# Kernel tuning notes

Hardware: AMD Instinct MI355X
Metric: run time of the kernel (lower is better)

Reference implementation:

```python
import jax, jax.numpy as jnp
import numpy as np

D_MODEL, D_INNER, D_CONV, D_STATE, DT_RANK = 1024, 2048, 4, 16, 64
B_SZ, L = 2, 2048


def setup_inputs() -> dict:
    key = jax.random.key(0)
    ks = jax.random.split(key, 8)
    s = 0.02
    x = jax.random.normal(ks[0], (B_SZ, L, D_MODEL), jnp.float32)
    in_proj_w = jax.random.normal(ks[1], (D_MODEL, 2 * D_INNER), jnp.float32) * s
    conv_w = jax.random.normal(ks[2], (D_INNER, 1, D_CONV), jnp.float32) * 0.1
    conv_b = jax.random.normal(ks[3], (D_INNER,), jnp.float32) * 0.1
    x_proj_w = jax.random.normal(ks[4], (D_INNER, DT_RANK + 2 * D_STATE), jnp.float32) * s
    dt_proj_w = jax.random.normal(ks[5], (DT_RANK, D_INNER), jnp.float32) * s
    dt_proj_b = jax.random.normal(ks[6], (D_INNER,), jnp.float32) * 0.1
    A_log = jnp.log(jnp.broadcast_to(jnp.arange(1, D_STATE + 1, dtype=jnp.float32), (D_INNER, D_STATE)))
    D = jnp.ones((D_INNER,), jnp.float32)
    out_proj_w = jax.random.normal(ks[7], (D_INNER, D_MODEL), jnp.float32) * s
    return dict(x=x, in_proj_w=in_proj_w, conv_w=conv_w, conv_b=conv_b,
                x_proj_w=x_proj_w, dt_proj_w=dt_proj_w, dt_proj_b=dt_proj_b,
                A_log=A_log, D=D, out_proj_w=out_proj_w)


def _selective_scan(u, delta, A, B, C, D):
    # u, delta: (b,l,d); A: (d,n); B,C: (b,l,n); D: (d,)
    b, l, d = u.shape
    n = A.shape[1]
    deltaA = jnp.exp(jnp.einsum('bld,dn->bldn', delta, A))          # (b,l,d,n)
    deltaB_u = jnp.einsum('bld,bln,bld->bldn', delta, B, u)          # (b,l,d,n)

    def step(xc, inputs):
        dA_t, dBu_t, C_t = inputs                                     # (b,d,n),(b,d,n),(b,n)
        xc = dA_t * xc + dBu_t
        y_t = jnp.einsum('bdn,bn->bd', xc, C_t)
        return xc, y_t

    x0 = jnp.zeros((b, d, n), u.dtype)
    _, ys = jax.lax.scan(step, x0, (deltaA.transpose(1, 0, 2, 3),
                                    deltaB_u.transpose(1, 0, 2, 3),
                                    C.transpose(1, 0, 2)))
    return ys.transpose(1, 0, 2) + u * D


def reference(x, in_proj_w, conv_w, conv_b, x_proj_w, dt_proj_w, dt_proj_b, A_log, D, out_proj_w):
    b, l, _ = x.shape
    xr = x @ in_proj_w                                                # (b,l,2*d_inner)
    xi, res = jnp.split(xr, 2, axis=-1)
    # causal depthwise conv1d (torch pads both sides by d_conv-1 then slices [:l])
    xc = jax.lax.conv_general_dilated(
        xi.transpose(0, 2, 1), conv_w, window_strides=(1,),
        padding=[(D_CONV - 1, 0)], feature_group_count=D_INNER,
        dimension_numbers=('NCH', 'OIH', 'NCH')) + conv_b[None, :, None]
    xc = jax.nn.silu(xc.transpose(0, 2, 1))                           # (b,l,d_inner)
    # SSM
    A = -jnp.exp(A_log)
    x_dbl = xc @ x_proj_w                                             # (b,l,dt_rank+2n)
    dt, Bm, Cm = jnp.split(x_dbl, [DT_RANK, DT_RANK + D_STATE], axis=-1)
    delta = jax.nn.softplus(dt @ dt_proj_w + dt_proj_b)               # (b,l,d_inner)
    y = _selective_scan(xc, delta, A, Bm, Cm, D)
    y = y * jax.nn.silu(res)
    return y @ out_proj_w
```

## Files before the change

### kernel.cpp

```cpp
#include <hip/hip_runtime.h>
#include <hip/hip_bf16.h>

#define D_MODEL 1024
#define D_INNER 2048
#define D_CONV  4
#define D_STATE 16
#define DT_RANK 64
#define B_SZ    2
#define SEQ_L   2048
#define BLROWS  (B_SZ * SEQ_L)

#define NCHUNK  64
#define CHUNK   (SEQ_L / NCHUNK)

#define XP_N    96
#define XP_SPLIT 8
#define XP_KCH  (D_INNER / XP_SPLIT)

typedef __hip_bfloat16 bf16;
typedef __attribute__((ext_vector_type(8))) short bshort8;
typedef __attribute__((ext_vector_type(4))) float f32x4;

__device__ __forceinline__ float b2f(bf16 v) { return __bfloat162float(v); }
__device__ __forceinline__ bf16  f2b(float v) { return __float2bfloat16(v); }
__device__ __forceinline__ short f2s(float v) {
    bf16 h = __float2bfloat16(v);
    return *reinterpret_cast<short*>(&h);
}
__device__ __forceinline__ float s2f(short s) {
    unsigned u = ((unsigned)(unsigned short)s) << 16;
    float f; __builtin_memcpy(&f, &u, 4); return f;
}
__device__ __forceinline__ float siluf(float x) { return x / (1.f + __expf(-x)); }
__device__ __forceinline__ float softplusf(float x) {
    return fmaxf(x, 0.f) + log1pf(__expf(-fabsf(x)));
}
__device__ __forceinline__ float exp_neg(float a) { return __expf(fminf(a, 0.f)); }

__device__ __forceinline__ void gl2lds16(const bf16* g, bf16* l) {
    __builtin_amdgcn_global_load_lds((const __attribute__((address_space(1))) void*)g,
                                     (__attribute__((address_space(3))) void*)l,
                                     16, 0, 0);
}

#define N_X    (B_SZ * SEQ_L * D_MODEL)
#define N_IPW  (D_MODEL * 2 * D_INNER)
#define N_CW   (D_INNER * D_CONV)
#define N_CB   (D_INNER)
#define N_XPW  (D_INNER * (DT_RANK + 2*D_STATE))
#define N_DTW  (DT_RANK * D_INNER)
#define N_DTB  (D_INNER)
#define N_AL   (D_INNER * D_STATE)
#define N_D    (D_INNER)
#define N_OPW  (D_INNER * D_MODEL)

#define S0 ((long)N_X)
#define S1 (S0 + N_IPW)
#define S2 (S1 + N_CW)
#define S3 (S2 + N_CB)
#define S4 (S3 + N_XPW)
#define S5 (S4 + N_DTW)
#define S6 (S5 + N_DTB)
#define S7 (S6 + N_AL)
#define S8 (S7 + N_D)
#define S9 (S8 + N_OPW)

#define PP_CVT   1024
#define PP_T0    4096
#define PP_T1    192
#define PP_T2    128
#define PP_T3    2048
#define PP_TOTAL (PP_CVT + PP_T0 + PP_T1 + PP_T2 + PP_T3)

__global__ __launch_bounds__(256)
void preprocess_kernel(int* __restrict__ flag,
                       const void* p0, const void* p1, const void* p2,
                       const void* p3, const void* p4, const void* p5,
                       const void* p6, const void* p7, const void* p8,
                       const void* p9,
                       bf16* __restrict__ canon,
                       bf16* __restrict__ d_ipw, bf16* __restrict__ d_xpw,
                       bf16* __restrict__ d_dtw, bf16* __restrict__ d_opw)
{
    __shared__ float tile[32][33];
    const float* al = (const float*)p7;
    const bool f32 = (fabsf(al[1] - 0.6931472f) < 0.05f) && (fabsf(al[0]) < 1e-3f);

    if (blockIdx.x == 0 && threadIdx.x == 0) {
        int fast = f32 ? 1 : 0;
        if (f32) {
            const int rows[3] = {0, 513, 1023};
            for (int i = 0; i < 3 && fast; ++i)
                for (int n = 0; n < D_STATE; ++n)
                    if (fabsf(al[rows[i] * D_STATE + n] - logf((float)(n + 1))) > 2e-3f)
                        { fast = 0; break; }
        }
        flag[0] = f32 ? 1 : 0;
        flag[1] = fast;
    }

    int bid = blockIdx.x;
    if (bid < PP_CVT) {
        const long total4 = S9 / 4;
        for (long i4 = (long)bid * 256 + threadIdx.x; i4 < total4;
             i4 += (long)PP_CVT * 256) {
            long idx = i4 * 4;
            const void* src; long lo; bool keep = true;
            if      (idx < S0) { src = p0; lo = idx; }
            else if (idx < S1) { src = p1; lo = idx - S0; keep = false; }
            else if (idx < S2) { src = p2; lo = idx - S1; }
            else if (idx < S3) { src = p3; lo = idx - S2; }
            else if (idx < S4) { src = p4; lo = idx - S3; keep = false; }
            else if (idx < S5) { src = p5; lo = idx - S4; keep = false; }
            else if (idx < S6) { src = p6; lo = idx - S5; }
            else if (idx < S7) { src = p7; lo = idx - S6; }
            else if (idx < S8) { src = p8; lo = idx - S7; }
            else               { src = p9; lo = idx - S8; keep = false; }
            if (!keep) continue;
            ushort4 o;
            if (f32) {
                float4 v = ((const float4*)src)[lo >> 2];
                o.x = (unsigned short)f2s(v.x); o.y = (unsigned short)f2s(v.y);
                o.z = (unsigned short)f2s(v.z); o.w = (unsigned short)f2s(v.w);
            } else {
                o = ((const ushort4*)src)[lo >> 2];
            }
            ((ushort4*)canon)[idx >> 2] = o;
        }
        return;
    }

    bid -= PP_CVT;
    const void* src; bf16* dst; int R, C, txt;
    if (bid < PP_T0)      { src = p1; dst = d_ipw; R = D_MODEL; C = 2 * D_INNER; txt = 128; }
    else if ((bid -= PP_T0) < PP_T1) { src = p4; dst = d_xpw; R = D_INNER; C = XP_N;    txt = 3;  }
    else if ((bid -= PP_T1) < PP_T2) { src = p5; dst = d_dtw; R = DT_RANK; C = D_INNER; txt = 64; }
    else                  { bid -= PP_T2; src = p9; dst = d_opw; R = D_INNER; C = D_MODEL; txt = 32; }

    const int r0 = (bid / txt) * 32, c0 = (bid % txt) * 32;
    const int tx = threadIdx.x & 31, ty = threadIdx.x >> 5;

    #pragma unroll
    for (int p = 0; p < 4; ++p) {
        int r = r0 + ty + p * 8, c = c0 + tx;
        float v = 0.f;
        if (r < R && c < C)
            v = f32 ? ((const float*)src)[(size_t)r * C + c]
                    : b2f(((const bf16*)src)[(size_t)r * C + c]);
        tile[ty + p * 8][tx] = v;
    }
    __syncthreads();
    #pragma unroll
    for (int p = 0; p < 4; ++p) {
        int c = c0 + ty + p * 8, r = r0 + tx;
        if (c < C && r < R)
            dst[(size_t)c * R + r] = f2b(tile[tx][ty + p * 8]);
    }
}

#define IP_NT (D_MODEL / 64)

#define IP_STA(nb, k0n, s)                                                    \
    { _Pragma("unroll") for (int c = 0; c < 2; ++c) {                         \
        const int rr = aR + (s) * 64 + c * 8;                                 \
        gl2lds16(A + (size_t)(row0 + rr + lr) * D_MODEL + (k0n) + slot * 8,   \
                 &As[nb][rr * 64]); } }

#define IP_STB(nb, k0n, s)                                                    \
    { _Pragma("unroll") for (int c = 0; c < 2; ++c) {                         \
        const int rr = bR + (s) * 16 + c * 8;                                 \
        gl2lds16(BT + (size_t)(col0 + rr + lr) * D_MODEL + (k0n) + slot * 8,  \
                 &Bs[nb][rr * 64]); } }

#define IP_LDB(cb)                                                            \
    { _Pragma("unroll") for (int j = 0; j < 4; ++j) {                         \
        bF[j][0] = *(const bshort8*)&Bs[cb][(wn*64 + j*16 + t15)*64 + fc0];   \
        bF[j][1] = *(const bshort8*)&Bs[cb][(wn*64 + j*16 + t15)*64 + fc1]; } }

#define IP_LDA(cb, i0)                                                        \
    { _Pragma("unroll") for (int ii = 0; ii < 2; ++ii) {                      \
        aF[ii][0] = *(const bshort8*)&As[cb][(wm*128 + ((i0)+ii)*16 + t15)*64 + fc0]; \
        aF[ii][1] = *(const bshort8*)&As[cb][(wm*128 + ((i0)+ii)*16 + t15)*64 + fc1]; } }

#define IP_MMA(i0)                                                            \
    __builtin_amdgcn_s_setprio(1);                                            \
    { _Pragma("unroll") for (int ii = 0; ii < 2; ++ii)                        \
      _Pragma("unroll") for (int j = 0; j < 4; ++j)                           \
      _Pragma("unroll") for (int h = 0; h < 2; ++h)                           \
        acc[(i0)+ii][j] = __builtin_amdgcn_mfma_f32_16x16x32_bf16(            \
            aF[ii][h], bF[j][h], acc[(i0)+ii][j], 0, 0, 0); }                 \
    __builtin_amdgcn_s_setprio(0);

__global__ __launch_bounds__(512, 2)
void gemm_inproj256_kernel(const bf16* __restrict__ A,
                           const bf16* __restrict__ BT,
                           bf16* __restrict__ C1,
                           bf16* __restrict__ C2)
{
    __shared__ __align__(16) bf16 As[2][256 * 64];
    __shared__ __align__(16) bf16 Bs[2][256 * 64];

    const int tid  = threadIdx.x;
    const int wave = tid >> 6;
    const int lane = tid & 63;
    const int t15  = lane & 15;
    const int q    = lane >> 4;
    const int wm   = wave >> 2;
    const int wn   = wave & 3;

    int wg = blockIdx.x;
    wg = (wg & 7) * 32 + (wg >> 3);
    const int row0 = (wg >> 4) * 256;
    const int col0 = (wg & 15) * 256;

    const int lr   = lane >> 3;
    const int slot = (lane & 7) ^ lr;
    const int aR   = wm * 128 + wn * 16;
    const int bR   = wn * 64  + wm * 32;
    const int x7   = t15 & 7;
    const int fc0  = ((0 + q) ^ x7) * 8;
    const int fc1  = ((4 + q) ^ x7) * 8;

    f32x4 acc[8][4] = {};
    bshort8 bF[4][2], aF[2][2];

    IP_STB(0, 0, 0); IP_STB(0, 0, 1); IP_STA(0, 0, 0); IP_STA(0, 0, 1);

    for (int t = 0; t < IP_NT - 1; ++t) {
        const int cb = t & 1, nb = cb ^ 1;
        const int k0n = (t + 1) * 64;
        asm volatile("s_waitcnt vmcnt(2)" ::: "memory");
        __builtin_amdgcn_s_barrier();
        __builtin_amdgcn_sched_barrier(0);
        IP_LDB(cb);
        IP_LDA(cb, 0);
        IP_STB(nb, k0n, 0);
        IP_MMA(0);
        IP_LDA(cb, 2);
        IP_STB(nb, k0n, 1);
        IP_MMA(2);
        asm volatile("s_waitcnt vmcnt(4)" ::: "memory");
        __builtin_amdgcn_s_barrier();
        __builtin_amdgcn_sched_barrier(0);
        IP_LDA(cb, 4);
        IP_STA(nb, k0n, 0);
        IP_MMA(4);
        IP_LDA(cb, 6);
        IP_STA(nb, k0n, 1);
        IP_MMA(6);
        asm volatile("s_waitcnt lgkmcnt(0)" ::: "memory");
    }
    {
        const int cb = (IP_NT - 1) & 1;
        asm volatile("s_waitcnt vmcnt(2)" ::: "memory");
        __builtin_amdgcn_s_barrier();
        __builtin_amdgcn_sched_barrier(0);
        IP_LDB(cb);
        IP_LDA(cb, 0); IP_MMA(0);
        IP_LDA(cb, 2); IP_MMA(2);
        asm volatile("s_waitcnt vmcnt(0)" ::: "memory");
        __builtin_amdgcn_s_barrier();
        __builtin_amdgcn_sched_barrier(0);
        IP_LDA(cb, 4); IP_MMA(4);
        IP_LDA(cb, 6); IP_MMA(6);
    }
    #pragma unroll
    for (int i = 0; i < 8; ++i) {
        #pragma unroll
        for (int j = 0; j < 4; ++j) {
            const int c_g = col0 + wn * 64 + j * 16 + t15;
            const int r_b = row0 + wm * 128 + i * 16 + q * 4;
            #pragma unroll
            for (int r = 0; r < 4; ++r) {
                const float v = acc[i][j][r];
                if (c_g < D_INNER)
                    C1[(size_t)(r_b + r) * D_INNER + c_g] = f2b(v);
                else
                    C2[(size_t)(r_b + r) * D_INNER + (c_g - D_INNER)] = f2b(v);
            }
        }
    }
}

__global__ __launch_bounds__(256)
void gemm_mfma_bt64_kernel(const bf16* __restrict__ A, int lda,
                           const bf16* __restrict__ BT, int ldb,
                           void* __restrict__ C, int ldc,
                           int M, int N, int K,
                           const bf16* __restrict__ bias, int mode,
                           const int* __restrict__ flag)
{
    __shared__ __align__(16) bf16 As[2][64 * 32];
    __shared__ __align__(16) bf16 Bs[2][128 * 32];

    const int tid  = threadIdx.x;
    const int wave = tid >> 6;
    const int lane = tid & 63;
    const int t    = lane & 15;
    const int q    = lane >> 4;
    const int wm   = wave & 1;
    const int wn   = wave >> 1;

    const int row0 = blockIdx.y * 64;
    const int col0 = blockIdx.x * 128;

    const int s_row = lane >> 2;
    const int s_col = (lane & 3) * 8;

    f32x4 acc[2][4] = {};
    const int outf32 = (mode == 2) ? flag[0] : 0;

    for (int k0 = 0; k0 < K; k0 += 64) {
        #pragma unroll
        for (int h = 0; h < 2; ++h) {
            if (wave < 2) {
                #pragma unroll
                for (int c = 0; c < 2; ++c) {
                    const bf16* g = A + (size_t)(row0 + wave * 32 + c * 16 + s_row) * lda
                                    + k0 + h * 32 + s_col;
                    gl2lds16(g, As[h] + (wave * 32 + c * 16) * 32);
                }
            } else {
                #pragma unroll
                for (int c = 0; c < 4; ++c) {
                    const bf16* g = BT + (size_t)(col0 + (wave - 2) * 64 + c * 16 + s_row) * ldb
                                    + k0 + h * 32 + s_col;
                    gl2lds16(g, Bs[h] + ((wave - 2) * 64 + c * 16) * 32);
                }
            }
        }
        __syncthreads();

        #pragma unroll
        for (int h = 0; h < 2; ++h) {
            bshort8 aF[2], bF[4];
            #pragma unroll
            for (int i = 0; i < 2; ++i)
                aF[i] = *(const bshort8*)&As[h][((wm * 32 + i * 16 + t) << 5) + (q << 3)];
            #pragma unroll
            for (int j = 0; j < 4; ++j)
                bF[j] = *(const bshort8*)&Bs[h][((wn * 64 + j * 16 + t) << 5) + (q << 3)];

            #pragma unroll
            for (int i = 0; i < 2; ++i)
                #pragma unroll
                for (int j = 0; j < 4; ++j)
                    acc[i][j] = __builtin_amdgcn_mfma_f32_16x16x32_bf16(
                                    aF[i], bF[j], acc[i][j], 0, 0, 0);
        }
        __syncthreads();
    }

    #pragma unroll
    for (int i = 0; i < 2; ++i) {
        #pragma unroll
        for (int j = 0; j < 4; ++j) {
            const int c_g = col0 + wn * 64 + j * 16 + t;
            const int r_b = row0 + wm * 32 + i * 16 + q * 4;
            #pragma unroll
            for (int r = 0; r < 4; ++r) {
                const int r_g = r_b + r;
                float v = acc[i][j][r];
                if (mode == 1) {
                    v += b2f(bias[c_g]);
                    ((bf16*)C)[(size_t)r_g * ldc + c_g] = f2b(softplusf(v));
                } else {
                    size_t o = (size_t)r_g * ldc + c_g;
                    if (outf32) ((float*)C)[o] = v;
                    else        ((bf16*)C)[o]  = f2b(v);
                }
            }
        }
    }
}

__global__ __launch_bounds__(256)
void xproj_splitk_kernel(const bf16* __restrict__ A,
                         const bf16* __restrict__ BT,
                         float* __restrict__ part)
{
    __shared__ __align__(16) bf16 As[2][128 * 32];
    __shared__ __align__(16) bf16 Bs[2][XP_N * 32];

    const int tid  = threadIdx.x;
    const int wave = tid >> 6;
    const int lane = tid & 63;
    const int t    = lane & 15;
    const int q    = lane >> 4;

    const int row0 = blockIdx.x * 128;
    const int s    = blockIdx.y;
    const int kbeg = s * XP_KCH;

    const int s_row = lane >> 2;
    const int s_col = (lane & 3) * 8;

    f32x4 acc[2][6] = {};

    for (int k0 = kbeg; k0 < kbeg + XP_KCH; k0 += 64) {
        #pragma unroll
        for (int h = 0; h < 2; ++h) {
            if (wave < 2) {
                #pragma unroll
                for (int c = 0; c < 4; ++c) {
                    const bf16* g = A + (size_t)(row0 + wave * 64 + c * 16 + s_row) * D_INNER
                                    + k0 + h * 32 + s_col;
                    gl2lds16(g, As[h] + (wave * 64 + c * 16) * 32);
                }
            } else {
                const int nb = (wave == 2) ? 4 : 2;
                for (int c = 0; c < nb; ++c) {
                    const bf16* g = BT + (size_t)((wave - 2) * 64 + c * 16 + s_row) * D_INNER
                                    + k0 + h * 32 + s_col;
                    gl2lds16(g, Bs[h] + ((wave - 2) * 64 + c * 16) * 32);
                }
            }
        }
        __syncthreads();

        #pragma unroll
        for (int h = 0; h < 2; ++h) {
            bshort8 aF[2], bF[6];
            #pragma unroll
            for (int i = 0; i < 2; ++i)
                aF[i] = *(const bshort8*)&As[h][((wave * 32 + i * 16 + t) << 5) + (q << 3)];
            #pragma unroll
            for (int j = 0; j < 6; ++j)
                bF[j] = *(const bshort8*)&Bs[h][((j * 16 + t) << 5) + (q << 3)];

            #pragma unroll
            for (int i = 0; i < 2; ++i)
                #pragma unroll
                for (int j = 0; j < 6; ++j)
                    acc[i][j] = __builtin_amdgcn_mfma_f32_16x16x32_bf16(
                                    aF[i], bF[j], acc[i][j], 0, 0, 0);
        }
        __syncthreads();
    }

    #pragma unroll
    for (int i = 0; i < 2; ++i) {
        #pragma unroll
        for (int j = 0; j < 6; ++j) {
            const int c_g = j * 16 + t;
            const int r_b = row0 + wave * 32 + i * 16 + q * 4;
            #pragma unroll
            for (int r = 0; r < 4; ++r)
                part[((size_t)s * BLROWS + (r_b + r)) * XP_N + c_g] = acc[i][j][r];
        }
    }
}

__global__ __launch_bounds__(256)
void xproj_reduce_kernel(const float* __restrict__ part, bf16* __restrict__ xdbl)
{
    int idx = blockIdx.x * 256 + threadIdx.x;
    if (idx >= BLROWS * XP_N) return;
    float v = 0.f;
    #pragma unroll
    for (int s = 0; s < XP_SPLIT; ++s)
        v += part[(size_t)s * BLROWS * XP_N + idx];
    xdbl[idx] = f2b(v);
}

__global__ __launch_bounds__(256)
void conv_silu_kernel(const bf16* __restrict__ xi,
                      const bf16* __restrict__ cw,
                      const bf16* __restrict__ cb,
                      bf16* __restrict__ xc)
{
    int idx = blockIdx.x * 256 + threadIdx.x;
    const int total = BLROWS * (D_INNER / 8);
    if (idx >= total) return;
    const int d8 = idx % (D_INNER / 8);
    const int bl = idx / (D_INNER / 8);
    const int l  = bl % SEQ_L;
    const int b  = bl / SEQ_L;
    const int d0 = d8 * 8;

    bshort8 cv[4];
    #pragma unroll
    for (int v = 0; v < 4; ++v)
        cv[v] = ((const bshort8*)(cw + (size_t)d0 * 4))[v];

    bshort8 bv = *(const bshort8*)(cb + d0);
    float acc[8];
    #pragma unroll
    for (int e = 0; e < 8; ++e) acc[e] = s2f(bv[e]);

    #pragma unroll
    for (int k = 0; k < D_CONV; ++k) {
        int tt = l + k - (D_CONV - 1);
        if (tt >= 0) {
            bshort8 xv = *(const bshort8*)(xi + ((size_t)b * SEQ_L + tt) * D_INNER + d0);
            #pragma unroll
            for (int e = 0; e < 8; ++e) {
                const int f = e * 4 + k;
                acc[e] += s2f(xv[e]) * s2f(cv[f >> 3][f & 7]);
            }
        }
    }
    bshort8 ov;
    #pragma unroll
    for (int e = 0; e < 8; ++e) {
        float a = acc[e];
        ov[e] = f2s(a * (1.f / (1.f + __expf(-a))));
    }
    *(bshort8*)(xc + (size_t)bl * D_INNER + d0) = ov;
}

__global__ __launch_bounds__(256)
void scan_p1_kernel(const bf16* delta, const bf16* xc, const bf16* xdbl,
                    const bf16* A_log,
                    float* state, float* sumdelta,
                    const int* flags)
{
    __shared__ float Bsh[CHUNK][D_STATE];
    const int tid = threadIdx.x;
    const int d = blockIdx.x * 256 + tid;
    const int c = blockIdx.y;
    const int b = blockIdx.z;
    const int row0 = b * SEQ_L + c * CHUNK;
    const int fastA = flags[1];

    for (int e = tid; e < CHUNK * D_STATE; e += 256) {
        int t = e / D_STATE, n = e % D_STATE;
        Bsh[t][n] = b2f(xdbl[(size_t)(row0 + t) * 96 + DT_RANK + n]);
    }
    __syncthreads();

    float A[D_STATE];
    if (!fastA) {
        #pragma unroll
        for (int n = 0; n < D_STATE; ++n) A[n] = -__expf(b2f(A_log[d * D_STATE + n]));
    }

    float x[D_STATE] = {};
    float S = 0.f;
    if (fastA) {
        for (int t = 0; t < CHUNK; ++t) {
            size_t r = row0 + t;
            float dt_v = b2f(delta[r * D_INNER + d]);
            float u    = b2f(xc[r * D_INNER + d]);
            float bu = dt_v * u;
            S += dt_v;
            float e1 = __expf(-fmaxf(dt_v, 0.f));
            float pw[D_STATE];
            pw[0] = e1;
            #pragma unroll
            for (int n = 1; n < D_STATE; ++n)
                pw[n] = pw[(n - 1) >> 1] * pw[n >> 1];
            #pragma unroll
            for (int n = 0; n < D_STATE; ++n)
                x[n] = pw[n] * x[n] + Bsh[t][n] * bu;
        }
    } else {
        for (int t = 0; t < CHUNK; ++t) {
            size_t r = row0 + t;
            float dt_v = b2f(delta[r * D_INNER + d]);
            float u    = b2f(xc[r * D_INNER + d]);
            float bu = dt_v * u;
            S += dt_v;
            #pragma unroll
            for (int n = 0; n < D_STATE; ++n)
                x[n] = exp_neg(dt_v * A[n]) * x[n] + Bsh[t][n] * bu;
        }
    }
    size_t o = ((size_t)(b * NCHUNK + c) * D_INNER + d) * D_STATE;
    #pragma unroll
    for (int n = 0; n < D_STATE; ++n) state[o + n] = x[n];
    sumdelta[(size_t)(b * NCHUNK + c) * D_INNER + d] = S;
}

__global__ __launch_bounds__(256)
void scan_p2_kernel(const bf16* A_log, float* state, const float* sumdelta)
{
    int idx = blockIdx.x * 256 + threadIdx.x;
    int n  = idx & (D_STATE - 1);
    int dn = idx >> 4;
    int d  = dn & (D_INNER - 1);
    int b  = dn >> 11;

    float A_n = -__expf(b2f(A_log[d * D_STATE + n]));
    float carry = 0.f;
    #pragma unroll 4
    for (int c = 0; c < NCHUNK; ++c) {
        size_t o = ((size_t)(b * NCHUNK + c) * D_INNER + d) * D_STATE + n;
        float local = state[o];
        float S = sumdelta[(size_t)(b * NCHUNK + c) * D_INNER + d];
        state[o] = carry;
        carry = exp_neg(A_n * S) * carry + local;
    }
}

__global__ __launch_bounds__(256)
void scan_p3_kernel(const bf16* delta, bf16* xc, const bf16* xdbl,
                    const bf16* res,
                    const bf16* A_log, const bf16* Dvec,
                    const float* state,
                    const int* flags)
{
    __shared__ float Bsh[CHUNK][D_STATE];
    __shared__ float Csh[CHUNK][D_STATE];
    const int tid = threadIdx.x;
    const int d = blockIdx.x * 256 + tid;
    const int c = blockIdx.y;
    const int b = blockIdx.z;
    const int row0 = b * SEQ_L + c * CHUNK;
    const int fastA = flags[1];

    for (int e = tid; e < CHUNK * 2 * D_STATE; e += 256) {
        int t = e / (2 * D_STATE), j = e % (2 * D_STATE);
        float v = b2f(xdbl[(size_t)(row0 + t) * 96 + DT_RANK + j]);
        if (j < D_STATE) Bsh[t][j] = v;
        else             Csh[t][j - D_STATE] = v;
    }
    __syncthreads();

    float A[D_STATE];
    if (!fastA) {
        #pragma unroll
        for (int n = 0; n < D_STATE; ++n) A[n] = -__expf(b2f(A_log[d * D_STATE + n]));
    }
    const float Dd = b2f(Dvec[d]);

    float x[D_STATE];
    size_t o = ((size_t)(b * NCHUNK + c) * D_INNER + d) * D_STATE;
    #pragma unroll
    for (int n = 0; n < D_STATE; ++n) x[n] = state[o + n];

    if (fastA) {
        for (int t = 0; t < CHUNK; ++t) {
            size_t r = row0 + t;
            float dt_v = b2f(delta[r * D_INNER + d]);
            float u    = b2f(xc[r * D_INNER + d]);
            float resv = b2f(res[r * D_INNER + d]);
            float bu = dt_v * u;
            float e1 = __expf(-fmaxf(dt_v, 0.f));
            float pw[D_STATE];
            pw[0] = e1;
            #pragma unroll
            for (int n = 1; n < D_STATE; ++n)
                pw[n] = pw[(n - 1) >> 1] * pw[n >> 1];
            float dot = 0.f;
            #pragma unroll
            for (int n = 0; n < D_STATE; ++n) {
                x[n] = pw[n] * x[n] + Bsh[t][n] * bu;
                dot += x[n] * Csh[t][n];
            }
            float y = (dot + u * Dd) * siluf(resv);
            xc[r * D_INNER + d] = f2b(y);
        }
    } else {
        for (int t = 0; t < CHUNK; ++t) {
            size_t r = row0 + t;
            float dt_v = b2f(delta[r * D_INNER + d]);
            float u    = b2f(xc[r * D_INNER + d]);
            float resv = b2f(res[r * D_INNER + d]);
            float bu = dt_v * u;
            float dot = 0.f;
            #pragma unroll
            for (int n = 0; n < D_STATE; ++n) {
                x[n] = exp_neg(dt_v * A[n]) * x[n] + Bsh[t][n] * bu;
                dot += x[n] * Csh[t][n];
            }
            float y = (dot + u * Dd) * siluf(resv);
            xc[r * D_INNER + d] = f2b(y);
        }
    }
}

extern "C" void kernel_launch(void* const* d_in, const int* in_sizes, int n_in,
                              void* d_out, int out_size, void* d_ws, size_t ws_size,
                              hipStream_t stream)
{
    char* ws = (char*)d_ws;
    int*  flag  = (int*)ws;
    bf16* canon = (bf16*)(ws + 64);

    bf16* c_x    = canon;
    bf16* c_ipwT = canon + S0;
    bf16* c_cw   = canon + S1;
    bf16* c_cb   = canon + S2;
    bf16* c_xpwT = canon + S3;
    bf16* c_dtwT = canon + S4;
    bf16* c_dtb  = canon + S5;
    bf16* c_al   = canon + S6;
    bf16* c_d    = canon + S7;
    bf16* c_opwT = canon + S8;

    char* p = ws + 64 + (size_t)S9 * sizeof(bf16);
    bf16* xi    = (bf16*)p;  p += (size_t)BLROWS * D_INNER * sizeof(bf16);
    bf16* xc    = (bf16*)p;  p += (size_t)BLROWS * D_INNER * sizeof(bf16);
    bf16* res   = (bf16*)p;  p += (size_t)BLROWS * D_INNER * sizeof(bf16);
    bf16* xdbl  = (bf16*)p;  p += (size_t)BLROWS * 96 * sizeof(bf16);
    bf16* delta = (bf16*)p;  p += (size_t)BLROWS * D_INNER * sizeof(bf16);
    float* sumdelta = (float*)p; p += (size_t)B_SZ * NCHUNK * D_INNER * 4;
    float* xp_part = (float*)xi;
    float* state   = (float*)xi;
    bf16* ybuf = xc;

    dim3 blk(256);

    preprocess_kernel<<<dim3(PP_TOTAL), blk, 0, stream>>>(
        flag, d_in[0], d_in[1], d_in[2], d_in[3], d_in[4],
        d_in[5], d_in[6], d_in[7], d_in[8], d_in[9],
        canon, c_ipwT, c_xpwT, c_dtwT, c_opwT);

    gemm_inproj256_kernel<<<dim3(256), dim3(512), 0, stream>>>(c_x, c_ipwT, xi, res);

    {
        int total = BLROWS * (D_INNER / 8);
        conv_silu_kernel<<<dim3((total + 255) / 256), blk, 0, stream>>>(xi, c_cw, c_cb, xc);
    }
    {
        dim3 g1(BLROWS / 128, XP_SPLIT);
        xproj_splitk_kernel<<<g1, blk, 0, stream>>>(xc, c_xpwT, xp_part);
        dim3 g2((BLROWS * XP_N) / 256);
        xproj_reduce_kernel<<<g2, blk, 0, stream>>>(xp_part, xdbl);
    }
    {
        dim3 g(D_INNER / 128, BLROWS / 64);
        gemm_mfma_bt64_kernel<<<g, blk, 0, stream>>>(xdbl, 96, c_dtwT, DT_RANK,
                                                     delta, D_INNER,
                                                     BLROWS, D_INNER, DT_RANK,
                                                     c_dtb, 1, flag);
    }
    {
        dim3 g1(D_INNER / 256, NCHUNK, B_SZ);
        scan_p1_kernel<<<g1, blk, 0, stream>>>(delta, xc, xdbl, c_al, state, sumdelta, flag);
        dim3 g2((B_SZ * D_INNER * D_STATE) / 256);
        scan_p2_kernel<<<g2, blk, 0, stream>>>(c_al, state, sumdelta);
        scan_p3_kernel<<<g1, blk, 0, stream>>>(delta, xc, xdbl, res, c_al, c_d, state, flag);
    }
    {
        dim3 g(D_MODEL / 128, BLROWS / 64);
        gemm_mfma_bt64_kernel<<<g, blk, 0, stream>>>(ybuf, D_INNER, c_opwT, D_INNER,
                                                     d_out, D_MODEL,
                                                     BLROWS, D_MODEL, D_INNER,
                                                     nullptr, 2, flag);
    }
}
```

Measured before the change: 309.5 us.

## Add split-K 256x128 tiled out-projection GEMM and prefetch scan inputs

Replaces the generic 64x128 out-projection GEMM with a dedicated 512-thread kernel. It uses 256x128 tiles, 64-wide K steps with XOR-swizzled LDS, direct global-to-LDS loads, double buffering, and a 2-way K split. A separate reduce kernel then sums the fp32 partials into the output. The scan pass-1 and pass-3 loops are also rewritten to load the next timestep's delta/u/res one iteration ahead, hiding global load latency. The split-K adds fp32 partial-buffer traffic and an extra launch, and it reuses the xi and delta workspace buffers for those partials.

```diff
diff --git a/kernel.cpp b/kernel.cpp
--- a/kernel.cpp
+++ b/kernel.cpp
@@ -282,6 +282,155 @@
     }
 }
 
+#define OP_NT 16
+
+#define OP_STB(nb, k0n)                                                       \
+    { _Pragma("unroll") for (int c = 0; c < 2; ++c) {                         \
+        const int rr = bRo + c * 8;                                           \
+        gl2lds16(BT + (size_t)(col0 + rr + lr) * D_INNER + (k0n) + slot * 8,  \
+                 &Bs[nb][rr * 64]); } }
+
+#define OP_STA1(nb, k0n)                                                      \
+    { _Pragma("unroll") for (int c = 0; c < 2; ++c) {                         \
+        const int rr = aRo1 + c * 8;                                          \
+        gl2lds16(A + (size_t)(row0 + rr + lr) * D_INNER + (k0n) + slot * 8,   \
+                 &As[nb][rr * 64]); } }
+
+#define OP_STA2(nb, k0n)                                                      \
+    { _Pragma("unroll") for (int c = 0; c < 2; ++c) {                         \
+        const int rr = aRo2 + c * 8;                                          \
+        gl2lds16(A + (size_t)(row0 + rr + lr) * D_INNER + (k0n) + slot * 8,   \
+                 &As[nb][rr * 64]); } }
+
+#define OP_LDB(cb)                                                            \
+    { _Pragma("unroll") for (int j = 0; j < 4; ++j) {                         \
+        bF[j][0] = *(const bshort8*)&Bs[cb][(wn*64 + j*16 + t15)*64 + fc0];   \
+        bF[j][1] = *(const bshort8*)&Bs[cb][(wn*64 + j*16 + t15)*64 + fc1]; } }
+
+#define OP_LDA(cb, p)                                                         \
+    { aF[0] = *(const bshort8*)&As[cb][(wm*64 + (p)*16 + t15)*64 + fc0];      \
+      aF[1] = *(const bshort8*)&As[cb][(wm*64 + (p)*16 + t15)*64 + fc1]; }
+
+#define OP_MMA(p)                                                             \
+    __builtin_amdgcn_s_setprio(1);                                            \
+    { _Pragma("unroll") for (int j = 0; j < 4; ++j)                           \
+      _Pragma("unroll") for (int h = 0; h < 2; ++h)                           \
+        acc[p][j] = __builtin_amdgcn_mfma_f32_16x16x32_bf16(                  \
+            aF[h], bF[j][h], acc[p][j], 0, 0, 0); }                           \
+    __builtin_amdgcn_s_setprio(0);
+
+__global__ __launch_bounds__(512, 2)
+void gemm_outproj_kernel(const bf16* __restrict__ A,
+                         const bf16* __restrict__ BT,
+                         float* __restrict__ part0,
+                         float* __restrict__ part1)
+{
+    __shared__ __align__(16) bf16 As[2][256 * 64];
+    __shared__ __align__(16) bf16 Bs[2][128 * 64];
+
+    const int tid  = threadIdx.x;
+    const int wave = tid >> 6;
+    const int lane = tid & 63;
+    const int t15  = lane & 15;
+    const int q    = lane >> 4;
+    const int wm   = wave >> 1;
+    const int wn   = wave & 1;
+
+    int wg = blockIdx.x;
+    wg = (wg & 7) * 32 + (wg >> 3);
+    const int s    = wg >> 7;
+    const int r    = wg & 127;
+    const int row0 = (r >> 3) * 256;
+    const int col0 = (r & 7) * 128;
+    const int kbeg = s * (D_INNER / 2);
+    float* __restrict__ part = s ? part1 : part0;
+
+    const int lr   = lane >> 3;
+    const int slot = (lane & 7) ^ lr;
+    const int bRo  = wn * 64 + wm * 16;
+    const int aRo1 = wm * 64 + wn * 16;
+    const int aRo2 = wm * 64 + 32 + wn * 16;
+    const int x7   = t15 & 7;
+    const int fc0  = ((0 + q) ^ x7) * 8;
+    const int fc1  = ((4 + q) ^ x7) * 8;
+
+    f32x4 acc[4][4] = {};
+    bshort8 bF[4][2], aF[2];
+
+    OP_STB(0, kbeg); OP_STA1(0, kbeg); OP_STA2(0, kbeg);
+
+    for (int kt = 0; kt < OP_NT - 1; ++kt) {
+        const int cb = kt & 1, nb = cb ^ 1;
+        const int k0n = kbeg + (kt + 1) * 64;
+        asm volatile("s_waitcnt vmcnt(2)" ::: "memory");
+        __builtin_amdgcn_s_barrier();
+        __builtin_amdgcn_sched_barrier(0);
+        OP_LDB(cb);
+        OP_LDA(cb, 0);
+        OP_STB(nb, k0n);
+        OP_MMA(0);
+        OP_LDA(cb, 1);
+        OP_STA1(nb, k0n);
+        OP_MMA(1);
+        asm volatile("s_waitcnt vmcnt(4)" ::: "memory");
+        __builtin_amdgcn_s_barrier();
+        __builtin_amdgcn_sched_barrier(0);
+        OP_LDA(cb, 2);
+        OP_STA2(nb, k0n);
+        OP_MMA(2);
+        OP_LDA(cb, 3);
+        OP_MMA(3);
+        asm volatile("s_waitcnt lgkmcnt(0)" ::: "memory");
+    }
+    {
+        const int cb = (OP_NT - 1) & 1;
+        asm volatile("s_waitcnt vmcnt(2)" ::: "memory");
+        __builtin_amdgcn_s_barrier();
+        __builtin_amdgcn_sched_barrier(0);
+        OP_LDB(cb);
+        OP_LDA(cb, 0); OP_MMA(0);
+        OP_LDA(cb, 1); OP_MMA(1);
+        asm volatile("s_waitcnt vmcnt(0)" ::: "memory");
+        __builtin_amdgcn_s_barrier();
+        __builtin_amdgcn_sched_barrier(0);
+        OP_LDA(cb, 2); OP_MMA(2);
+        OP_LDA(cb, 3); OP_MMA(3);
+    }
+    #pragma unroll
+    for (int i = 0; i < 4; ++i) {
+        #pragma unroll
+        for (int j = 0; j < 4; ++j) {
+            const int c_g = col0 + wn * 64 + j * 16 + t15;
+            const int r_b = row0 + wm * 64 + i * 16 + q * 4;
+            #pragma unroll
+            for (int rr2 = 0; rr2 < 4; ++rr2)
+                part[(size_t)(r_b + rr2) * D_MODEL + c_g] = acc[i][j][rr2];
+        }
+    }
+}
+
+__global__ __launch_bounds__(256)
+void outproj_reduce_kernel(const float* __restrict__ p0,
+                           const float* __restrict__ p1,
+                           void* __restrict__ out,
+                           const int* __restrict__ flag)
+{
+    const int i = blockIdx.x * 256 + threadIdx.x;
+    const int total = BLROWS * D_MODEL / 4;
+    if (i >= total) return;
+    float4 a = ((const float4*)p0)[i];
+    float4 b = ((const float4*)p1)[i];
+    float4 v = make_float4(a.x + b.x, a.y + b.y, a.z + b.z, a.w + b.w);
+    if (flag[0]) {
+        ((float4*)out)[i] = v;
+    } else {
+        ushort4 o;
+        o.x = (unsigned short)f2s(v.x); o.y = (unsigned short)f2s(v.y);
+        o.z = (unsigned short)f2s(v.z); o.w = (unsigned short)f2s(v.w);
+        ((ushort4*)out)[i] = o;
+    }
+}
+
 __global__ __launch_bounds__(256)
 void gemm_mfma_bt64_kernel(const bf16* __restrict__ A, int lda,
                            const bf16* __restrict__ BT, int ldb,
@@ -538,13 +687,19 @@
     float x[D_STATE] = {};
     float S = 0.f;
     if (fastA) {
+        const bf16* dp = delta + (size_t)row0 * D_INNER + d;
+        const bf16* up = xc    + (size_t)row0 * D_INNER + d;
+        float dt_c = b2f(dp[0]);
+        float u_c  = b2f(up[0]);
         for (int t = 0; t < CHUNK; ++t) {
-            size_t r = row0 + t;
-            float dt_v = b2f(delta[r * D_INNER + d]);
-            float u    = b2f(xc[r * D_INNER + d]);
-            float bu = dt_v * u;
-            S += dt_v;
-            float e1 = __expf(-fmaxf(dt_v, 0.f));
+            float dt_n = 0.f, u_n = 0.f;
+            if (t + 1 < CHUNK) {
+                dt_n = b2f(dp[(size_t)(t + 1) * D_INNER]);
+                u_n  = b2f(up[(size_t)(t + 1) * D_INNER]);
+            }
+            float bu = dt_c * u_c;
+            S += dt_c;
+            float e1 = __expf(-fmaxf(dt_c, 0.f));
             float pw[D_STATE];
             pw[0] = e1;
             #pragma unroll
@@ -553,6 +708,7 @@
             #pragma unroll
             for (int n = 0; n < D_STATE; ++n)
                 x[n] = pw[n] * x[n] + Bsh[t][n] * bu;
+            dt_c = dt_n; u_c = u_n;
         }
     } else {
         for (int t = 0; t < CHUNK; ++t) {
@@ -630,13 +786,21 @@
     for (int n = 0; n < D_STATE; ++n) x[n] = state[o + n];
 
     if (fastA) {
+        const bf16* dp = delta + (size_t)row0 * D_INNER + d;
+        const bf16* up = xc    + (size_t)row0 * D_INNER + d;
+        const bf16* rp = res   + (size_t)row0 * D_INNER + d;
+        float dt_c = b2f(dp[0]);
+        float u_c  = b2f(up[0]);
+        float re_c = b2f(rp[0]);
         for (int t = 0; t < CHUNK; ++t) {
-            size_t r = row0 + t;
-            float dt_v = b2f(delta[r * D_INNER + d]);
-            float u    = b2f(xc[r * D_INNER + d]);
-            float resv = b2f(res[r * D_INNER + d]);
-            float bu = dt_v * u;
-            float e1 = __expf(-fmaxf(dt_v, 0.f));
+            float dt_n = 0.f, u_n = 0.f, re_n = 0.f;
+            if (t + 1 < CHUNK) {
+                dt_n = b2f(dp[(size_t)(t + 1) * D_INNER]);
+                u_n  = b2f(up[(size_t)(t + 1) * D_INNER]);
+                re_n = b2f(rp[(size_t)(t + 1) * D_INNER]);
+            }
+            float bu = dt_c * u_c;
+            float e1 = __expf(-fmaxf(dt_c, 0.f));
             float pw[D_STATE];
             pw[0] = e1;
             #pragma unroll
@@ -648,8 +812,9 @@
                 x[n] = pw[n] * x[n] + Bsh[t][n] * bu;
                 dot += x[n] * Csh[t][n];
             }
-            float y = (dot + u * Dd) * siluf(resv);
-            xc[r * D_INNER + d] = f2b(y);
+            float y = (dot + u_c * Dd) * siluf(re_c);
+            xc[(size_t)(row0 + t) * D_INNER + d] = f2b(y);
+            dt_c = dt_n; u_c = u_n; re_c = re_n;
         }
     } else {
         for (int t = 0; t < CHUNK; ++t) {
@@ -698,6 +863,8 @@
     float* sumdelta = (float*)p; p += (size_t)B_SZ * NCHUNK * D_INNER * 4;
     float* xp_part = (float*)xi;
     float* state   = (float*)xi;
+    float* part_o0 = (float*)xi;
+    float* part_o1 = (float*)delta;
     bf16* ybuf = xc;
 
     dim3 blk(256);
@@ -734,10 +901,9 @@
         scan_p3_kernel<<<g1, blk, 0, stream>>>(delta, xc, xdbl, res, c_al, c_d, state, flag);
     }
     {
-        dim3 g(D_MODEL / 128, BLROWS / 64);
-        gemm_mfma_bt64_kernel<<<g, blk, 0, stream>>>(ybuf, D_INNER, c_opwT, D_INNER,
-                                                     d_out, D_MODEL,
-                                                     BLROWS, D_MODEL, D_INNER,
-                                                     nullptr, 2, flag);
-    }
-}
+        gemm_outproj_kernel<<<dim3(256), dim3(512), 0, stream>>>(ybuf, c_opwT,
+                                                                 part_o0, part_o1);
+        outproj_reduce_kernel<<<dim3((BLROWS * D_MODEL / 4) / 256), blk, 0, stream>>>(
+            part_o0, part_o1, d_out, flag);
+    }
+}
```

Result: faster. 300.7 us (-2.8%).
